# Performance work log

Hardware: AMD Instinct MI355X
Metric: run time of the kernel (lower is better)

The kernel has to match this reference:

```python
import jax, jax.numpy as jnp
import numpy as np
import math

# Config (mirrors LlamaConfig passed to __init__)
V = 32000      # vocab_size
D = 1024       # n_embd
H = 16         # n_head
KVH = 4        # n_key_value_heads
R = H // KVH   # repeat_kv_heads = 4
HD = D // H    # head_size = 64
L = 4          # n_layer
I = 2730       # n_intermediate = 1024*4*2//3
T_CTX = 1024   # n_ctx / block_size
RD = HD        # rotary_dim = n_embd // n_head (full head rotated)
BASE = 10000.0 # rotary_base
EPS = 1e-6


def rope_sin_cos(T):
    # GPT-NeoX style (rotary_adjacent_pairs=False): freq repeated twice
    pos = jnp.arange(T, dtype=jnp.float32)
    dim = jnp.arange(RD // 2, dtype=jnp.float32)
    freq = BASE ** (dim / (RD / 2))
    freq = jnp.concatenate([freq, freq])          # (RD,)
    ang = pos[:, None] / freq[None, :]            # (T, RD)
    return jnp.sin(ang), jnp.cos(ang)


def apply_rope(x, sin, cos):
    # x: (B, H, T, HD); rotate_every_two with halves: [x0, x1] -> [-x1, x0]
    n = RD // 2
    flip = jnp.concatenate([-x[..., n:], x[..., :n]], axis=-1)
    return x * cos[None, None, :, :] + flip * sin[None, None, :, :]


def rmsnorm(x, w):
    xf = x.astype(jnp.float32)
    var = jnp.mean(xf * xf, axis=-1, keepdims=True)
    return w * (xf * jax.lax.rsqrt(var + EPS)).astype(x.dtype)


def attention(x, Wq, Wkv, Wo, sin, cos):
    B, T, C = x.shape
    kv = x @ Wkv.T                                 # (B, T, 2*C/R)
    k, v = jnp.split(kv, 2, axis=-1)               # each (B, T, KVH*HD)
    q = x @ Wq.T                                   # (B, T, C)
    # torch repeat_interleave(dim=1)+view(B,T,H,HD) == q head h reads kv head (h % KVH)
    k = jnp.tile(k.reshape(B, T, KVH, HD), (1, 1, R, 1)).transpose(0, 2, 1, 3)  # (B,H,T,HD)
    v = jnp.tile(v.reshape(B, T, KVH, HD), (1, 1, R, 1)).transpose(0, 2, 1, 3)
    q = q.reshape(B, T, H, HD).transpose(0, 2, 1, 3)
    q = apply_rope(q, sin, cos)
    k = apply_rope(k, sin, cos)
    scores = jnp.einsum('bhqd,bhkd->bhqk', q, k) * (1.0 / math.sqrt(HD))
    causal = jnp.tril(jnp.ones((T, T), dtype=bool))
    scores = jnp.where(causal[None, None], scores, -jnp.inf)
    att = jax.nn.softmax(scores, axis=-1)
    y = jnp.einsum('bhqk,bhkd->bhqd', att, v)
    y = y.transpose(0, 2, 1, 3).reshape(B, T, C)
    return y @ Wo.T


def swiglu(x, Wg, Wu, Wd):
    return (jax.nn.silu(x @ Wg.T) * (x @ Wu.T)) @ Wd.T


def setup_inputs() -> dict:
    key = jax.random.key(0)
    ks = jax.random.split(key, 10)
    std = 0.02
    res_std = 0.02 / math.sqrt(2 * L)  # LLMC_RESIDUAL_SCALE_FLAG projections
    wte = jax.random.normal(ks[0], (V, D), jnp.float32) * std
    Wq = jax.random.normal(ks[1], (L, D, D), jnp.float32) * std
    Wkv = jax.random.normal(ks[2], (L, 2 * D // R, D), jnp.float32) * std
    Wo = jax.random.normal(ks[3], (L, D, D), jnp.float32) * res_std
    Wg = jax.random.normal(ks[4], (L, I, D), jnp.float32) * std
    Wu = jax.random.normal(ks[5], (L, I, D), jnp.float32) * std
    Wd = jax.random.normal(ks[6], (L, D, I), jnp.float32) * res_std
    rms1 = jnp.ones((L, D), jnp.float32)
    rms2 = jnp.ones((L, D), jnp.float32)
    rms_f = jnp.ones((D,), jnp.float32)
    idx = jax.random.randint(ks[7], (2, 1024), 0, V, dtype=jnp.int64 if jax.config.jax_enable_x64 else jnp.int32)
    return dict(idx=idx, wte=wte, Wq=Wq, Wkv=Wkv, Wo=Wo, Wg=Wg, Wu=Wu, Wd=Wd,
                rms1=rms1, rms2=rms2, rms_f=rms_f)


def reference(idx, wte, Wq, Wkv, Wo, Wg, Wu, Wd, rms1, rms2, rms_f):
    B, T = idx.shape
    sin, cos = rope_sin_cos(T)
    x = wte[idx]                                   # (B, T, D)
    for l in range(L):
        x = x + attention(rmsnorm(x, rms1[l]), Wq[l], Wkv[l], Wo[l], sin, cos)
        x = x + swiglu(rmsnorm(x, rms2[l]), Wg[l], Wu[l], Wd[l])
    x = rmsnorm(x, rms_f)
    logits = x @ wte.T                             # tied lm_head
    return logits
```

## Files before the change

kernel.cpp:

```cpp
#include <hip/hip_runtime.h>
#include <hip/hip_bf16.h>
#include <math.h>

#define BB 2
#define TT 1024
#define DD 1024
#define NH 16
#define KVHN 4
#define NL 4
#define II 2730
#define IIP 2816
#define NTOK (BB * TT)
#define QKVD 1536
#define KSTR 72

typedef __hip_bfloat16 bf16;
typedef __attribute__((ext_vector_type(8))) short bf16x8;
typedef __attribute__((ext_vector_type(4))) float f32x4;

#define GLOAD16(gp, lp)                                                        \
    __builtin_amdgcn_global_load_lds(                                          \
        (const __attribute__((address_space(1))) unsigned int*)(gp),           \
        (__attribute__((address_space(3))) unsigned int*)(lp), 16, 0, 0)

__device__ inline float b2f(unsigned short u) {
    union { unsigned int i; float f; } v;
    v.i = (unsigned int)u << 16;
    return v.f;
}
__device__ inline unsigned short f2b(float f) {
    __hip_bfloat16 b = __float2bfloat16(f);
    return *(unsigned short*)&b;
}

__global__ void rope_table_k(float* __restrict__ st, float* __restrict__ ct) {
    int i = blockIdx.x * 256 + threadIdx.x;
    if (i >= TT * 64) return;
    int t = i >> 6, d = i & 63;
    float freq = powf(10000.0f, (float)(d & 31) / 32.0f);
    float ang = (float)t / freq;
    st[i] = sinf(ang);
    ct[i] = cosf(ang);
}

__global__ __launch_bounds__(256) void embed_k(const int* __restrict__ idx,
                                               const float* __restrict__ wte,
                                               float* __restrict__ x) {
    int row = blockIdx.x;
    int tok = idx[row];
    const float4* src = (const float4*)(wte + (size_t)tok * DD);
    float4* dst = (float4*)(x + (size_t)row * DD);
    dst[threadIdx.x] = src[threadIdx.x];
}

__global__ __launch_bounds__(256) void rmsnorm_k(const float* __restrict__ x,
                                                 const float* __restrict__ w,
                                                 bf16* __restrict__ o) {
    int row = blockIdx.x;
    float4 v = ((const float4*)(x + (size_t)row * DD))[threadIdx.x];
    float s = v.x * v.x + v.y * v.y + v.z * v.z + v.w * v.w;
#pragma unroll
    for (int off = 32; off > 0; off >>= 1) s += __shfl_down(s, off);
    __shared__ float red[4];
    if ((threadIdx.x & 63) == 0) red[threadIdx.x >> 6] = s;
    __syncthreads();
    float tot = red[0] + red[1] + red[2] + red[3];
    float r = rsqrtf(tot * (1.0f / DD) + 1e-6f);
    float4 wv = ((const float4*)w)[threadIdx.x];
    size_t base = (size_t)row * DD + threadIdx.x * 4;
    ushort4 ov;
    ov.x = f2b(v.x * r * wv.x);
    ov.y = f2b(v.y * r * wv.y);
    ov.z = f2b(v.z * r * wv.z);
    ov.w = f2b(v.w * r * wv.w);
    *(ushort4*)(o + base) = ov;
}

__global__ __launch_bounds__(256) void pack_v_k(const bf16* __restrict__ vb,
                                                bf16* __restrict__ vt) {
    int t0 = blockIdx.x * 64;
    int kvh = blockIdx.y;
    int b = blockIdx.z;
    __shared__ unsigned short Ls[64][65];
    int tid = threadIdx.x;
    const unsigned short* vbs = (const unsigned short*)vb;
    unsigned short* vts = (unsigned short*)vt;
    for (int e = tid; e < 64 * 64; e += 256) {
        int tl = e >> 6, d = e & 63;
        Ls[tl][d] = vbs[((size_t)(b * KVHN + kvh) * TT + t0 + tl) * 64 + d];
    }
    __syncthreads();
    for (int e = tid; e < 64 * 64; e += 256) {
        int d = e >> 6, tl = e & 63;
        vts[((size_t)(b * KVHN + kvh) * 64 + d) * TT + t0 + tl] = Ls[tl][d];
    }
}

__global__ __launch_bounds__(256) void attn_mfma_k(const bf16* __restrict__ qp,
                                                   const bf16* __restrict__ kp,
                                                   const bf16* __restrict__ vt,
                                                   bf16* __restrict__ y) {
    int qt = blockIdx.x;
    int h = blockIdx.y;
    int b = blockIdx.z;
    int kvh = h & (KVHN - 1);

    __shared__ __align__(16) bf16 Ks[64][KSTR];
    __shared__ __align__(16) bf16 Vt[64][KSTR];
    __shared__ __align__(16) bf16 Ps[4][16][KSTR];

    int tid = threadIdx.x;
    int lane = tid & 63;
    int w = tid >> 6;
    int qi = lane & 15;
    int g = lane >> 4;

    const bf16* qbase = qp + (((size_t)(b * NH + h) * TT + qt * 64 + w * 16 + qi) * 64);
    bf16x8 qf0 = *(const bf16x8*)(qbase + g * 8);
    bf16x8 qf1 = *(const bf16x8*)(qbase + 32 + g * 8);

    const bf16* kg = kp + ((size_t)(b * KVHN + kvh) * TT) * 64;
    const bf16* vg = vt + ((size_t)(b * KVHN + kvh) * 64) * TT;

    f32x4 oacc[4] = {};
    float m = -INFINITY, l = 0.0f;
    int qglob = qt * 64 + w * 16 + qi;

    for (int kt = 0; kt <= qt; ++kt) {
        __syncthreads();
        {
            int c0 = tid, c1 = tid + 256;
            *(bf16x8*)(&Ks[c0 >> 3][(c0 & 7) * 8]) =
                *(const bf16x8*)(kg + (size_t)(kt * 64 + (c0 >> 3)) * 64 + (c0 & 7) * 8);
            *(bf16x8*)(&Ks[c1 >> 3][(c1 & 7) * 8]) =
                *(const bf16x8*)(kg + (size_t)(kt * 64 + (c1 >> 3)) * 64 + (c1 & 7) * 8);
            *(bf16x8*)(&Vt[c0 >> 3][(c0 & 7) * 8]) =
                *(const bf16x8*)(vg + (size_t)(c0 >> 3) * TT + kt * 64 + (c0 & 7) * 8);
            *(bf16x8*)(&Vt[c1 >> 3][(c1 & 7) * 8]) =
                *(const bf16x8*)(vg + (size_t)(c1 >> 3) * TT + kt * 64 + (c1 & 7) * 8);
        }
        __syncthreads();

        f32x4 sacc[4] = {};
#pragma unroll
        for (int stt = 0; stt < 4; ++stt) {
            bf16x8 kf0 = *(const bf16x8*)(&Ks[stt * 16 + qi][g * 8]);
            bf16x8 kf1 = *(const bf16x8*)(&Ks[stt * 16 + qi][32 + g * 8]);
            sacc[stt] = __builtin_amdgcn_mfma_f32_16x16x32_bf16(kf0, qf0, sacc[stt], 0, 0, 0);
            sacc[stt] = __builtin_amdgcn_mfma_f32_16x16x32_bf16(kf1, qf1, sacc[stt], 0, 0, 0);
        }

        if (kt == qt) {
#pragma unroll
            for (int stt = 0; stt < 4; ++stt)
#pragma unroll
                for (int r = 0; r < 4; ++r) {
                    int kgl = kt * 64 + stt * 16 + g * 4 + r;
                    if (kgl > qglob) sacc[stt][r] = -INFINITY;
                }
        }

        float tmax = -INFINITY;
#pragma unroll
        for (int stt = 0; stt < 4; ++stt)
#pragma unroll
            for (int r = 0; r < 4; ++r) tmax = fmaxf(tmax, sacc[stt][r]);
        tmax = fmaxf(tmax, __shfl_xor(tmax, 16));
        tmax = fmaxf(tmax, __shfl_xor(tmax, 32));
        float mnew = fmaxf(m, tmax);
        float scale = __expf(m - mnew);
        float psum = 0.0f;
#pragma unroll
        for (int stt = 0; stt < 4; ++stt) {
            bf16 pb[4];
#pragma unroll
            for (int r = 0; r < 4; ++r) {
                float p = __expf(sacc[stt][r] - mnew);
                psum += p;
                pb[r] = __float2bfloat16(p);
            }
            *(uint2*)(&Ps[w][qi][stt * 16 + g * 4]) = *(uint2*)pb;
        }
        psum += __shfl_xor(psum, 16);
        psum += __shfl_xor(psum, 32);
        l = l * scale + psum;
        m = mnew;

        float sc0 = __shfl(scale, g * 4 + 0);
        float sc1 = __shfl(scale, g * 4 + 1);
        float sc2 = __shfl(scale, g * 4 + 2);
        float sc3 = __shfl(scale, g * 4 + 3);
#pragma unroll
        for (int dt = 0; dt < 4; ++dt) {
            oacc[dt][0] *= sc0; oacc[dt][1] *= sc1;
            oacc[dt][2] *= sc2; oacc[dt][3] *= sc3;
        }

#pragma unroll
        for (int kc = 0; kc < 2; ++kc) {
            bf16x8 pa = *(const bf16x8*)(&Ps[w][qi][kc * 32 + g * 8]);
#pragma unroll
            for (int dt = 0; dt < 4; ++dt) {
                bf16x8 vb2 = *(const bf16x8*)(&Vt[dt * 16 + qi][kc * 32 + g * 8]);
                oacc[dt] = __builtin_amdgcn_mfma_f32_16x16x32_bf16(pa, vb2, oacc[dt], 0, 0, 0);
            }
        }
    }

    float linv = 1.0f / l;
    float li0 = __shfl(linv, g * 4 + 0);
    float li1 = __shfl(linv, g * 4 + 1);
    float li2 = __shfl(linv, g * 4 + 2);
    float li3 = __shfl(linv, g * 4 + 3);
#pragma unroll
    for (int dt = 0; dt < 4; ++dt) {
        int dcol = h * 64 + dt * 16 + qi;
        size_t r0 = (size_t)(b * TT + qt * 64 + w * 16 + g * 4) * DD + dcol;
        y[r0 + 0 * DD] = __float2bfloat16(oacc[dt][0] * li0);
        y[r0 + 1 * DD] = __float2bfloat16(oacc[dt][1] * li1);
        y[r0 + 2 * DD] = __float2bfloat16(oacc[dt][2] * li2);
        y[r0 + 3 * DD] = __float2bfloat16(oacc[dt][3] * li3);
    }
}

__device__ inline void cvt_body(const float* __restrict__ src, bf16* __restrict__ dst,
                                int Msrc, int Ksrc, int Kdst, int total4,
                                int rmul, int radd, int start, int stride) {
    for (int i4 = start; i4 < total4; i4 += stride) {
        int i = i4 * 4;
        int r = i / Kdst, c = i - r * Kdst;
        ushort4 o;
        if (r < Msrc && c + 4 <= Ksrc && (Ksrc & 3) == 0) {
            float4 v = *(const float4*)(src + (size_t)r * Ksrc + c);
            o.x = f2b(v.x); o.y = f2b(v.y); o.z = f2b(v.z); o.w = f2b(v.w);
        } else {
            float v0 = (r < Msrc && c + 0 < Ksrc) ? src[(size_t)r * Ksrc + c + 0] : 0.0f;
            float v1 = (r < Msrc && c + 1 < Ksrc) ? src[(size_t)r * Ksrc + c + 1] : 0.0f;
            float v2 = (r < Msrc && c + 2 < Ksrc) ? src[(size_t)r * Ksrc + c + 2] : 0.0f;
            float v3 = (r < Msrc && c + 3 < Ksrc) ? src[(size_t)r * Ksrc + c + 3] : 0.0f;
            o.x = f2b(v0); o.y = f2b(v1); o.z = f2b(v2); o.w = f2b(v3);
        }
        *(ushort4*)(dst + ((size_t)(r * rmul + radd) * Kdst + c)) = o;
    }
}

__global__ void cvt_pad_k(const float* __restrict__ src, bf16* __restrict__ dst,
                          int Msrc, int Ksrc, int Kdst, int total4) {
    cvt_body(src, dst, Msrc, Ksrc, Kdst, total4, 1, 0,
             blockIdx.x * 256 + threadIdx.x, gridDim.x * 256);
}

struct CvtJobs {
    const float* src[6];
    bf16* dst[6];
    int Msrc[6], Ksrc[6], Kdst[6], n4[6], rmul[6], radd[6];
};
__global__ void cvt_fused_k(CvtJobs j) {
    int job = blockIdx.y;
    cvt_body(j.src[job], j.dst[job], j.Msrc[job], j.Ksrc[job], j.Kdst[job],
             j.n4[job], j.rmul[job], j.radd[job],
             blockIdx.x * 256 + threadIdx.x, gridDim.x * 256);
}

template <int MODE, int BM, int BN>
__global__ __launch_bounds__(256) void gemm_bt(const bf16* __restrict__ A,
                                               const bf16* __restrict__ W16,
                                               const float* res, void* Cv,
                                               int N, int M, int K,
                                               const float* __restrict__ st,
                                               const float* __restrict__ ct,
                                               bf16* qp, bf16* kp, bf16* vb) {
    constexpr int MF = BM / 32;
    constexpr int NF = BN / 32;
    __shared__ __align__(16) bf16 As[BM * 32];
    __shared__ __align__(16) bf16 Bs[BN * 32];

    int t = threadIdx.x;
    int nnt = N / BM;
    int nmt = M / BN;
    int nwg = nmt * nnt;
    int orig = blockIdx.x;
    int q8 = nwg >> 3;
    int wgid = (orig & 7) * q8 + (orig >> 3);
    int mt, nt;
    if constexpr (BM == 128 && BN == 128) {
        int stile = wgid >> 5, rem = wgid & 31;
        mt = (stile << 1) + (rem & 1);
        nt = rem >> 1;
    } else {
        mt = wgid / nnt;
        nt = wgid - mt * nnt;
    }
    int m0 = mt * BN;
    int n0 = nt * BM;

    int lane = t & 63;
    int wave = t >> 6;
    int wr = (wave >> 1) * (BM / 2);
    int wc = (wave & 1) * (BN / 2);
    int qi = lane & 15;
    int g4 = lane >> 4;

    const bf16* gA1 = A + (size_t)(n0 + (t >> 2)) * K + ((t & 3) * 8);
    const bf16* gA2 = A + (size_t)(n0 + ((t + 256) >> 2)) * K + ((t & 3) * 8);
    const bf16* gB1 = W16 + (size_t)(m0 + (t >> 2)) * K + ((t & 3) * 8);
    const bf16* gB2 = W16 + (size_t)(m0 + ((t + 256) >> 2)) * K + ((t & 3) * 8);

    f32x4 acc[MF][NF] = {};

    for (int k0 = 0; k0 < K; k0 += 32) {
        __syncthreads();
        GLOAD16(gA1 + k0, As + t * 8);
        if constexpr (BM == 128) GLOAD16(gA2 + k0, As + (t + 256) * 8);
        GLOAD16(gB1 + k0, Bs + t * 8);
        if constexpr (BN == 128) GLOAD16(gB2 + k0, Bs + (t + 256) * 8);
        __syncthreads();

        bf16x8 af[MF], bfr[NF];
#pragma unroll
        for (int m = 0; m < MF; m++)
            af[m] = *(const bf16x8*)(As + (wr + m * 16 + qi) * 32 + g4 * 8);
#pragma unroll
        for (int n = 0; n < NF; n++)
            bfr[n] = *(const bf16x8*)(Bs + (wc + n * 16 + qi) * 32 + g4 * 8);
#pragma unroll
        for (int m = 0; m < MF; m++)
#pragma unroll
            for (int n = 0; n < NF; n++)
                acc[m][n] = __builtin_amdgcn_mfma_f32_16x16x32_bf16(af[m], bfr[n], acc[m][n], 0, 0, 0);
    }

    int colb = m0 + wc + qi;
    int rowb = n0 + wr + g4 * 4;

    if constexpr (MODE == 0) {
        float* Cf = (float*)Cv;
#pragma unroll
        for (int m = 0; m < MF; m++) {
#pragma unroll
            for (int n = 0; n < NF; n++) {
#pragma unroll
                for (int r = 0; r < 4; r++) {
                    size_t off = (size_t)(rowb + m * 16 + r) * M + (colb + n * 16);
                    __builtin_nontemporal_store(acc[m][n][r], Cf + off);
                }
            }
        }
    } else if constexpr (MODE == 1) {
        float* Cf = (float*)Cv;
#pragma unroll
        for (int m = 0; m < MF; m++) {
#pragma unroll
            for (int n = 0; n < NF; n++) {
#pragma unroll
                for (int r = 0; r < 4; r++) {
                    size_t off = (size_t)(rowb + m * 16 + r) * M + (colb + n * 16);
                    Cf[off] = acc[m][n][r] + res[off];
                }
            }
        }
    } else if constexpr (MODE == 3) {
        bf16* Cb = (bf16*)Cv;
        int M2 = M >> 1;
        bool even = (lane & 1) == 0;
#pragma unroll
        for (int m = 0; m < MF; m++) {
#pragma unroll
            for (int n = 0; n < NF; n++) {
#pragma unroll
                for (int r = 0; r < 4; r++) {
                    float own = acc[m][n][r];
                    float oth = __shfl_xor(own, 1);
                    if (even) {
                        float sv = own / (1.0f + __expf(-own)) * oth;
                        int oc = (colb + n * 16) >> 1;
                        Cb[(size_t)(rowb + m * 16 + r) * M2 + oc] = __float2bfloat16(sv);
                    }
                }
            }
        }
    } else if constexpr (MODE == 4) {
        int h = (m0 + wc) >> 6;
#pragma unroll
        for (int m = 0; m < MF; m++) {
#pragma unroll
            for (int r = 0; r < 4; r++) {
                int row = rowb + m * 16 + r;
                int tt = row & (TT - 1);
                int b = row >> 10;
                if (h < 20) {
#pragma unroll
                    for (int n = 0; n < 2; n++) {
                        int dlo = qi + n * 16;
                        float alo = acc[m][n][r];
                        float ahi = acc[m][n + 2][r];
                        float c = ct[tt * 64 + dlo];
                        float s = st[tt * 64 + dlo];
                        float olo = alo * c - ahi * s;
                        float ohi = ahi * c + alo * s;
                        if (h < 16) {
                            olo *= 0.125f; ohi *= 0.125f;
                            bf16* q = qp + (((size_t)(b * NH + h) * TT + tt) * 64);
                            q[dlo] = __float2bfloat16(olo);
                            q[dlo + 32] = __float2bfloat16(ohi);
                        } else {
                            bf16* kk = kp + (((size_t)(b * KVHN + (h - 16)) * TT + tt) * 64);
                            kk[dlo] = __float2bfloat16(olo);
                            kk[dlo + 32] = __float2bfloat16(ohi);
                        }
                    }
                } else {
                    bf16* vv = vb + (((size_t)(b * KVHN + (h - 20)) * TT + tt) * 64);
#pragma unroll
                    for (int n = 0; n < 4; n++)
                        vv[qi + n * 16] = __float2bfloat16(acc[m][n][r]);
                }
            }
        }
    }
}

extern "C" void kernel_launch(void* const* d_in, const int* in_sizes, int n_in,
                              void* d_out, int out_size, void* d_ws, size_t ws_size,
                              hipStream_t stream) {
    const int* idx    = (const int*)d_in[0];
    const float* wte  = (const float*)d_in[1];
    const float* Wq   = (const float*)d_in[2];
    const float* Wkv  = (const float*)d_in[3];
    const float* Wo   = (const float*)d_in[4];
    const float* Wg   = (const float*)d_in[5];
    const float* Wu   = (const float*)d_in[6];
    const float* Wd   = (const float*)d_in[7];
    const float* rms1 = (const float*)d_in[8];
    const float* rms2 = (const float*)d_in[9];
    const float* rmsf = (const float*)d_in[10];
    float* out = (float*)d_out;

    char* ws = (char*)d_ws;
    size_t off = 0;
    float* x = (float*)(ws + off);   off += (size_t)NTOK * DD * 4;
    bf16* xn = (bf16*)(ws + off);    off += (size_t)NTOK * DD * 2;
    float* st = (float*)(ws + off);  off += (size_t)TT * 64 * 4;
    float* ct = (float*)(ws + off);  off += (size_t)TT * 64 * 4;
    bf16* yb = (bf16*)(ws + off);    off += (size_t)NTOK * DD * 2;
    bf16* gb = (bf16*)(ws + off);    off += (size_t)NTOK * IIP * 2;
    bf16* qp = (bf16*)(ws + off);    off += (size_t)NTOK * DD * 2;
    bf16* kp = (bf16*)(ws + off);    off += (size_t)BB * KVHN * TT * 64 * 2;
    bf16* vb = (bf16*)(ws + off);    off += (size_t)BB * KVHN * TT * 64 * 2;
    bf16* vt = (bf16*)(ws + off);    off += (size_t)BB * KVHN * TT * 64 * 2;
    bf16* Wqkv_buf = (bf16*)(ws + off); off += (size_t)QKVD * DD * 2;
    bf16* Wo_buf = (bf16*)(ws + off);   off += (size_t)DD * DD * 2;
    bf16* Wgu_buf = (bf16*)(ws + off);  off += (size_t)2 * IIP * DD * 2;
    bf16* Wd_buf = (bf16*)(ws + off);   off += (size_t)DD * IIP * 2;
    bf16* wte_bf = (bf16*)(ws + off);   off += (size_t)32000 * DD * 2;

    rope_table_k<<<(TT * 64 + 255) / 256, 256, 0, stream>>>(st, ct);
    embed_k<<<NTOK, 256, 0, stream>>>(idx, wte, x);

    for (int l = 0; l < NL; ++l) {
        CvtJobs j;
        j.src[0] = Wq + (size_t)l * DD * DD;   j.dst[0] = Wqkv_buf;
        j.Msrc[0] = DD;  j.Ksrc[0] = DD;  j.Kdst[0] = DD;  j.n4[0] = DD * DD / 4;
        j.rmul[0] = 1; j.radd[0] = 0;
        j.src[1] = Wkv + (size_t)l * 512 * DD; j.dst[1] = Wqkv_buf + (size_t)DD * DD;
        j.Msrc[1] = 512; j.Ksrc[1] = DD;  j.Kdst[1] = DD;  j.n4[1] = 512 * DD / 4;
        j.rmul[1] = 1; j.radd[1] = 0;
        j.src[2] = Wo + (size_t)l * DD * DD;   j.dst[2] = Wo_buf;
        j.Msrc[2] = DD;  j.Ksrc[2] = DD;  j.Kdst[2] = DD;  j.n4[2] = DD * DD / 4;
        j.rmul[2] = 1; j.radd[2] = 0;
        j.src[3] = Wg + (size_t)l * II * DD;   j.dst[3] = Wgu_buf;
        j.Msrc[3] = II;  j.Ksrc[3] = DD;  j.Kdst[3] = DD;  j.n4[3] = IIP * DD / 4;
        j.rmul[3] = 2; j.radd[3] = 0;
        j.src[4] = Wu + (size_t)l * II * DD;   j.dst[4] = Wgu_buf;
        j.Msrc[4] = II;  j.Ksrc[4] = DD;  j.Kdst[4] = DD;  j.n4[4] = IIP * DD / 4;
        j.rmul[4] = 2; j.radd[4] = 1;
        j.src[5] = Wd + (size_t)l * DD * II;   j.dst[5] = Wd_buf;
        j.Msrc[5] = DD;  j.Ksrc[5] = II;  j.Kdst[5] = IIP; j.n4[5] = DD * IIP / 4;
        j.rmul[5] = 1; j.radd[5] = 0;
        cvt_fused_k<<<dim3(512, 6), 256, 0, stream>>>(j);

        rmsnorm_k<<<NTOK, 256, 0, stream>>>(x, rms1 + (size_t)l * DD, xn);
        gemm_bt<4, 64, 128><<<(QKVD / 128) * (NTOK / 64), 256, 0, stream>>>(
            xn, Wqkv_buf, nullptr, nullptr, NTOK, QKVD, DD, st, ct, qp, kp, vb);
        pack_v_k<<<dim3(TT / 64, KVHN, BB), 256, 0, stream>>>(vb, vt);
        attn_mfma_k<<<dim3(TT / 64, NH, BB), 256, 0, stream>>>(qp, kp, vt, yb);
        gemm_bt<1, 64, 64><<<(DD / 64) * (NTOK / 64), 256, 0, stream>>>(
            yb, Wo_buf, x, x, NTOK, DD, DD, nullptr, nullptr, nullptr, nullptr, nullptr);
        rmsnorm_k<<<NTOK, 256, 0, stream>>>(x, rms2 + (size_t)l * DD, xn);
        gemm_bt<3, 128, 128><<<(2 * IIP / 128) * (NTOK / 128), 256, 0, stream>>>(
            xn, Wgu_buf, nullptr, gb, NTOK, 2 * IIP, DD, nullptr, nullptr, nullptr, nullptr, nullptr);
        gemm_bt<1, 64, 64><<<(DD / 64) * (NTOK / 64), 256, 0, stream>>>(
            gb, Wd_buf, x, x, NTOK, DD, IIP, nullptr, nullptr, nullptr, nullptr, nullptr);
    }

    rmsnorm_k<<<NTOK, 256, 0, stream>>>(x, rmsf, xn);
    cvt_pad_k<<<2048, 256, 0, stream>>>(wte, wte_bf, 32000, DD, DD, 32000 * DD / 4);
    gemm_bt<0, 128, 128><<<(32000 / 128) * (NTOK / 128), 256, 0, stream>>>(
        xn, wte_bf, nullptr, out, NTOK, 32000, DD, nullptr, nullptr, nullptr, nullptr, nullptr);
}
```

Baseline: 928.6 us.

## Add triple-buffered 512-thread pipelined GEMM for LM head projection

Replaces the generic gemm_bt for the tied LM head (2048x32000x1024) with a dedicated kernel. It uses 256x128 tiles, 8 waves, a three-stage LDS ring filled by direct global-to-LDS loads with an XOR swizzle, and explicit vmcnt waits so the next K tiles load while MFMAs run. It also remaps workgroup IDs for cache locality, raises wave priority around the MFMA block, and writes results with nontemporal stores. The cost is 144 KB of dynamic LDS per block, which allows only one block per CU, and more reliance on hand-placed barriers for correctness.

```diff
diff --git a/kernel.cpp b/kernel.cpp
--- a/kernel.cpp
+++ b/kernel.cpp
@@ -420,6 +420,114 @@
     }
 }
 
+__global__ __launch_bounds__(512) void gemm_pipe_k(const bf16* __restrict__ A,
+                                                   const bf16* __restrict__ W,
+                                                   float* __restrict__ C, int M) {
+    extern __shared__ __align__(16) char lds[];
+    const int NKT = DD / 64;
+
+    int t = threadIdx.x;
+    int lane = t & 63;
+    int w = t >> 6;
+    int wm = w >> 2;
+    int wn = w & 3;
+    int qi = lane & 15;
+    int g4 = lane >> 4;
+
+    int nnt = NTOK / 256;
+    int nwg = (M / 128) * nnt;
+    int orig = blockIdx.x;
+    int wgid = (orig & 7) * (nwg >> 3) + (orig >> 3);
+    int mt = wgid / nnt;
+    int nt = wgid - mt * nnt;
+    int m0 = mt * 128;
+    int n0 = nt * 256;
+
+    int wr = wm * 128;
+    int wcn = wn * 32;
+
+    f32x4 acc[8][2] = {};
+
+    auto stage = [&](int kt, char* buf, int th) {
+#pragma unroll
+        for (int c = 0; c < 2; c++) {
+            int p = th * 16384 + c * 8192 + t * 16;
+            int row = p >> 7;
+            int scb = (p & 127) ^ ((row & 7) << 4);
+            GLOAD16(A + (size_t)(n0 + row) * DD + kt * 64 + (scb >> 1), buf + p);
+        }
+        {
+            int p = th * 8192 + t * 16;
+            int row = p >> 7;
+            int scb = (p & 127) ^ ((row & 7) << 4);
+            GLOAD16(W + (size_t)(m0 + row) * DD + kt * 64 + (scb >> 1), buf + 32768 + p);
+        }
+    };
+
+    stage(0, lds, 0);
+    stage(0, lds, 1);
+    stage(1, lds + 49152, 0);
+    stage(1, lds + 49152, 1);
+    asm volatile("s_waitcnt vmcnt(6)" ::: "memory");
+    __builtin_amdgcn_s_barrier();
+
+    int bsel = 0;
+    for (int j = 0; j < NKT; ++j) {
+        char* buf = lds + bsel * 49152;
+        int snext = bsel + 2;
+        if (snext >= 3) snext -= 3;
+        char* sbuf = lds + snext * 49152;
+        bool dost = (j + 2) < NKT;
+#pragma unroll
+        for (int p = 0; p < 2; ++p) {
+            bf16x8 af[8], bfrag[2];
+            int cb = p * 64 + g4 * 16;
+#pragma unroll
+            for (int m = 0; m < 8; m++) {
+                int r = wr + m * 16 + qi;
+                af[m] = *(const bf16x8*)(buf + r * 128 + (cb ^ ((r & 7) << 4)));
+            }
+#pragma unroll
+            for (int n = 0; n < 2; n++) {
+                int rb = wcn + n * 16 + qi;
+                bfrag[n] = *(const bf16x8*)(buf + 32768 + rb * 128 + (cb ^ ((rb & 7) << 4)));
+            }
+            if (dost) stage(j + 2, sbuf, p);
+            if (p == 1) {
+                if (j <= NKT - 3) {
+                    asm volatile("s_waitcnt vmcnt(6)" ::: "memory");
+                } else {
+                    asm volatile("s_waitcnt vmcnt(0)" ::: "memory");
+                }
+            }
+            __builtin_amdgcn_s_barrier();
+            asm volatile("s_waitcnt lgkmcnt(0)" ::: "memory");
+            __builtin_amdgcn_sched_barrier(0);
+            __builtin_amdgcn_s_setprio(1);
+#pragma unroll
+            for (int m = 0; m < 8; m++)
+#pragma unroll
+                for (int n = 0; n < 2; n++)
+                    acc[m][n] = __builtin_amdgcn_mfma_f32_16x16x32_bf16(af[m], bfrag[n], acc[m][n], 0, 0, 0);
+            __builtin_amdgcn_s_setprio(0);
+            __builtin_amdgcn_s_barrier();
+        }
+        bsel += 1;
+        if (bsel >= 3) bsel -= 3;
+    }
+
+#pragma unroll
+    for (int m = 0; m < 8; m++)
+#pragma unroll
+        for (int n = 0; n < 2; n++)
+#pragma unroll
+            for (int r = 0; r < 4; r++) {
+                size_t off = (size_t)(n0 + wr + m * 16 + g4 * 4 + r) * M +
+                             (m0 + wcn + n * 16 + qi);
+                __builtin_nontemporal_store(acc[m][n][r], C + off);
+            }
+}
+
 extern "C" void kernel_launch(void* const* d_in, const int* in_sizes, int n_in,
                               void* d_out, int out_size, void* d_ws, size_t ws_size,
                               hipStream_t stream) {
@@ -435,6 +543,9 @@
     const float* rms2 = (const float*)d_in[9];
     const float* rmsf = (const float*)d_in[10];
     float* out = (float*)d_out;
+
+    hipFuncSetAttribute(reinterpret_cast<const void*>(&gemm_pipe_k),
+                        hipFuncAttributeMaxDynamicSharedMemorySize, 147456);
 
     char* ws = (char*)d_ws;
     size_t off = 0;
@@ -495,6 +606,6 @@
 
     rmsnorm_k<<<NTOK, 256, 0, stream>>>(x, rmsf, xn);
     cvt_pad_k<<<2048, 256, 0, stream>>>(wte, wte_bf, 32000, DD, DD, 32000 * DD / 4);
-    gemm_bt<0, 128, 128><<<(32000 / 128) * (NTOK / 128), 256, 0, stream>>>(
-        xn, wte_bf, nullptr, out, NTOK, 32000, DD, nullptr, nullptr, nullptr, nullptr, nullptr);
-}
+    gemm_pipe_k<<<(32000 / 128) * (NTOK / 256), 512, 147456, stream>>>(
+        xn, wte_bf, out, 32000);
+}
```

New measurement: 915.7 us. About the same (-1.4%).

## Double GEMM K-step to 64 with XOR-swizzled LDS layout

Applied to the files above, without the earlier changes.

The bf16 GEMM now stages 64-wide K slices per iteration instead of 32, which halves the number of barrier pairs per tile and doubles the MFMA work between syncs. Shared-memory tiles use 128-byte rows with an XOR swizzle on 16-byte chunks, applied on the global-load source address, to avoid LDS bank conflicts on the fragment reads. LDS use doubles, which may lower occupancy, and all K dimensions must be multiples of 64.

```diff
diff --git a/kernel.cpp b/kernel.cpp
--- a/kernel.cpp
+++ b/kernel.cpp
@@ -272,8 +272,10 @@
                                                bf16* qp, bf16* kp, bf16* vb) {
     constexpr int MF = BM / 32;
     constexpr int NF = BN / 32;
-    __shared__ __align__(16) bf16 As[BM * 32];
-    __shared__ __align__(16) bf16 Bs[BN * 32];
+    constexpr int ACH = BM / 32;
+    constexpr int BCH = BN / 32;
+    __shared__ __align__(16) bf16 As[BM * 64];
+    __shared__ __align__(16) bf16 Bs[BN * 64];
 
     int t = threadIdx.x;
     int nnt = N / BM;
@@ -301,33 +303,57 @@
     int qi = lane & 15;
     int g4 = lane >> 4;
 
-    const bf16* gA1 = A + (size_t)(n0 + (t >> 2)) * K + ((t & 3) * 8);
-    const bf16* gA2 = A + (size_t)(n0 + ((t + 256) >> 2)) * K + ((t & 3) * 8);
-    const bf16* gB1 = W16 + (size_t)(m0 + (t >> 2)) * K + ((t & 3) * 8);
-    const bf16* gB2 = W16 + (size_t)(m0 + ((t + 256) >> 2)) * K + ((t & 3) * 8);
+    int arow[ACH], asc[ACH], apos[ACH];
+#pragma unroll
+    for (int i = 0; i < ACH; i++) {
+        int p = (t + i * 256) * 16;
+        arow[i] = p >> 7;
+        asc[i] = (p & 127) ^ ((arow[i] & 7) << 4);
+        apos[i] = p;
+    }
+    int brow[BCH], bsc[BCH], bpos[BCH];
+#pragma unroll
+    for (int i = 0; i < BCH; i++) {
+        int p = (t + i * 256) * 16;
+        brow[i] = p >> 7;
+        bsc[i] = (p & 127) ^ ((brow[i] & 7) << 4);
+        bpos[i] = p;
+    }
 
     f32x4 acc[MF][NF] = {};
 
-    for (int k0 = 0; k0 < K; k0 += 32) {
+    for (int k0 = 0; k0 < K; k0 += 64) {
         __syncthreads();
-        GLOAD16(gA1 + k0, As + t * 8);
-        if constexpr (BM == 128) GLOAD16(gA2 + k0, As + (t + 256) * 8);
-        GLOAD16(gB1 + k0, Bs + t * 8);
-        if constexpr (BN == 128) GLOAD16(gB2 + k0, Bs + (t + 256) * 8);
+#pragma unroll
+        for (int i = 0; i < ACH; i++)
+            GLOAD16(A + (size_t)(n0 + arow[i]) * K + k0 + (asc[i] >> 1),
+                    (char*)As + apos[i]);
+#pragma unroll
+        for (int i = 0; i < BCH; i++)
+            GLOAD16(W16 + (size_t)(m0 + brow[i]) * K + k0 + (bsc[i] >> 1),
+                    (char*)Bs + bpos[i]);
         __syncthreads();
 
-        bf16x8 af[MF], bfr[NF];
-#pragma unroll
-        for (int m = 0; m < MF; m++)
-            af[m] = *(const bf16x8*)(As + (wr + m * 16 + qi) * 32 + g4 * 8);
-#pragma unroll
-        for (int n = 0; n < NF; n++)
-            bfr[n] = *(const bf16x8*)(Bs + (wc + n * 16 + qi) * 32 + g4 * 8);
-#pragma unroll
-        for (int m = 0; m < MF; m++)
-#pragma unroll
-            for (int n = 0; n < NF; n++)
-                acc[m][n] = __builtin_amdgcn_mfma_f32_16x16x32_bf16(af[m], bfr[n], acc[m][n], 0, 0, 0);
+#pragma unroll
+        for (int h = 0; h < 2; h++) {
+            int cb = h * 64 + g4 * 16;
+            bf16x8 af[MF], bfr[NF];
+#pragma unroll
+            for (int m = 0; m < MF; m++) {
+                int r = wr + m * 16 + qi;
+                af[m] = *(const bf16x8*)((const char*)As + r * 128 + (cb ^ ((r & 7) << 4)));
+            }
+#pragma unroll
+            for (int n = 0; n < NF; n++) {
+                int r = wc + n * 16 + qi;
+                bfr[n] = *(const bf16x8*)((const char*)Bs + r * 128 + (cb ^ ((r & 7) << 4)));
+            }
+#pragma unroll
+            for (int m = 0; m < MF; m++)
+#pragma unroll
+                for (int n = 0; n < NF; n++)
+                    acc[m][n] = __builtin_amdgcn_mfma_f32_16x16x32_bf16(af[m], bfr[n], acc[m][n], 0, 0, 0);
+        }
     }
 
     int colb = m0 + wc + qi;
```

New measurement: 855.2 us. 7.9% less time.
